# Kernel tuning notes

Measured on AMD Instinct MI355X. Metric: run time of the kernel, lower is better.

Reference implementation:

```python
import jax, jax.numpy as jnp
import numpy as np

WS = 7       # window_size
NH = 4       # num_head = dim_in // dim_head
HD = 64      # dim_head
ALPHA = 0.1
BETA = 0.2
THETA = 0.5
EPS = 1e-5   # LayerNorm eps


def dwconv(x, w):
    # x: [b, C, h, w], w: [C, 1, k, k] depthwise, padding 'same', no bias
    return jax.lax.conv_general_dilated(
        x, w, window_strides=(1, 1), padding='SAME',
        feature_group_count=x.shape[1],
        dimension_numbers=('NCHW', 'OIHW', 'NCHW'))


def setup_inputs() -> dict:
    key = jax.random.key(0)
    ks = jax.random.split(key, 8)
    B, H, W, C = 32, 56, 56, 256
    s = 0.02
    return {
        'x': jax.random.normal(ks[0], (B, H, W, C), jnp.float32),
        'qkv_w': jax.random.normal(ks[1], (3 * C, C), jnp.float32) * s,
        'qkv_b': jnp.zeros((3 * C,), jnp.float32),
        'conv3_w': jax.random.normal(ks[2], (C, 1, 3, 3), jnp.float32) * s,
        'conv5_w': jax.random.normal(ks[3], (C, 1, 5, 5), jnp.float32) * s,
        'conv7_w': jax.random.normal(ks[4], (C, 1, 7, 7), jnp.float32) * s,
        'ffn_in_w': jax.random.normal(ks[5], (C, C), jnp.float32) * s,
        'ffn_out_w': jax.random.normal(ks[6], (C, C), jnp.float32) * s,
        'ln_g': jnp.ones((C,), jnp.float32),
        'ln_b': jnp.zeros((C,), jnp.float32),
    }


def reference(x, qkv_w, qkv_b, conv3_w, conv5_w, conv7_w, ffn_in_w, ffn_out_w, ln_g, ln_b):
    B, H, W, C = x.shape
    n1, n2 = H // WS, W // WS  # H,W divisible by WS -> no padding path
    # rearrange 'b (h1 n1) (w1 n2) c -> (b n1 n2) h1 w1 c' (window dim is MAJOR axis)
    xw = x.reshape(B, WS, n1, WS, n2, C).transpose(0, 2, 4, 1, 3, 5)
    xw = xw.reshape(B * n1 * n2, WS, WS, C)
    b, hw = B * n1 * n2, WS * WS

    shortcut = xw.reshape(b, hw, NH, HD).transpose(0, 2, 1, 3)  # [b, nh, hw, hd]
    qkv = xw.reshape(b, hw, C) @ qkv_w.T + qkv_b                # [b, hw, 3C]
    qkv = qkv.reshape(b, hw, 3, NH, HD).transpose(2, 0, 3, 1, 4)
    q, k, v = qkv[0], qkv[1], qkv[2]
    v = ALPHA * v + shortcut                                     # scaled residual into V
    shortcut2 = v.transpose(0, 2, 1, 3).reshape(b, WS, WS, C)    # [b, h, w, C]

    # SDPA with default scale hd^-0.5
    attn = jax.nn.softmax(jnp.einsum('bnqd,bnkd->bnqk', q, k) * (HD ** -0.5), axis=-1)
    x_spa = jnp.einsum('bnqk,bnkd->bnqd', attn, v)
    x_spa = x_spa.transpose(0, 2, 1, 3).reshape(b, WS, WS, C)

    # conv branches on modified v: v.transpose(-1,-2).reshape(b, C, h, w)
    xc = v.transpose(0, 1, 3, 2).reshape(b, C, WS, WS)
    c3 = dwconv(xc, conv3_w).transpose(0, 2, 3, 1)
    c5 = dwconv(xc, conv5_w).transpose(0, 2, 3, 1)
    c7 = dwconv(xc, conv7_w).transpose(0, 2, 3, 1)
    x_spa = 0.25 * (x_spa + c3 + c5 + c7)  # equal 0.25 branch weights

    xw = BETA * x_spa + shortcut2
    # inverse rearrange '(b n1 n2) h1 w1 c -> b (h1 n1) (w1 n2) c'
    xo = xw.reshape(B, n1, n2, WS, WS, C).transpose(0, 3, 1, 4, 2, 5).reshape(B, H, W, C)

    # FFN (bias=False) with scaled residual, then LayerNorm
    y = jax.nn.silu(xo @ ffn_in_w.T) @ ffn_out_w.T
    xo = THETA * y + xo
    mu = jnp.mean(xo, axis=-1, keepdims=True)
    var = jnp.var(xo, axis=-1, keepdims=True)
    return (xo - mu) / jnp.sqrt(var + EPS) * ln_g + ln_b
```

## Files before the change

### kernel.cpp

```cpp
#include <hip/hip_runtime.h>

typedef unsigned short u16;
typedef unsigned short u16x8 __attribute__((ext_vector_type(8)));
typedef unsigned short u16x4 __attribute__((ext_vector_type(4)));
typedef unsigned int   u32x2 __attribute__((ext_vector_type(2)));
typedef short          s16x8 __attribute__((ext_vector_type(8)));
typedef float          f32x4 __attribute__((ext_vector_type(4)));

#define DEV static __device__ __forceinline__

DEV float bf2f(u16 u){ unsigned int v = ((unsigned int)u) << 16; return __builtin_bit_cast(float, v); }
DEV u16 f2bf(float f){
  unsigned int u = __builtin_bit_cast(unsigned int, f);
  u += 0x7fffu + ((u >> 16) & 1u);
  return (u16)(u >> 16);
}

DEV f32x4 mfma16(u16x8 a, u16x8 b, f32x4 c){
  return __builtin_amdgcn_mfma_f32_16x16x32_bf16(
      __builtin_bit_cast(s16x8, a), __builtin_bit_cast(s16x8, b), c, 0, 0, 0);
}

DEV void g2l16(const void* g, void* l){
  __builtin_amdgcn_global_load_lds((const __attribute__((address_space(1))) void*)g,
                                   (__attribute__((address_space(3))) void*)l, 16, 0, 0);
}

DEV size_t xrow_from(int b, int hw){
  int h1 = hw / 7, w1 = hw - h1 * 7;
  return ((size_t)(((b >> 6) * 56 + h1 * 8 + ((b >> 3) & 7)) * 56 + (w1 * 8 + (b & 7)))) << 8;
}
DEV size_t xrow_off(int t){ int b = t / 49; return xrow_from(b, t - b * 49); }

DEV size_t xo_off(int t, int ch){
  int b = t / 49, hw = t - b * 49;
  return (size_t)b * 12544 + (size_t)((ch >> 7) * 6272) + (size_t)hw * 128 + (ch & 127);
}

__global__ __launch_bounds__(256) void k_prep(const float* __restrict__ qkvw,
                                              const float* __restrict__ c3,
                                              const float* __restrict__ c5,
                                              const float* __restrict__ c7,
                                              const float* __restrict__ fin,
                                              const float* __restrict__ fout,
                                              u16* __restrict__ wq, u16* __restrict__ wfi,
                                              u16* __restrict__ wfo, float* __restrict__ weff){
  int id = blockIdx.x * 256 + threadIdx.x;
  if (id < 196608) { wq[id] = f2bf(qkvw[id]); return; }
  id -= 196608;
  if (id < 65536) { wfi[id] = f2bf(fin[id]); return; }
  id -= 65536;
  if (id < 65536) { wfo[id] = f2bf(fout[id]); return; }
  id -= 65536;
  if (id < 12544) {
    int c = id / 49, t = id - c * 49;
    int di = t / 7 - 3, dj = t % 7 - 3;
    float s = c7[c * 49 + t];
    if (di >= -2 && di <= 2 && dj >= -2 && dj <= 2) s += c5[c * 25 + (di + 2) * 5 + (dj + 2)];
    if (di >= -1 && di <= 1 && dj >= -1 && dj <= 1) s += c3[c * 9 + (di + 1) * 3 + (dj + 1)];
    weff[t * 256 + c] = 0.05f * s;
  }
}

__global__ __launch_bounds__(256) void k_xbf(const float* __restrict__ x, u16* __restrict__ xbf){
  int tid = threadIdx.x;
  int tok = blockIdx.x * 4 + (tid >> 6);
  int c4 = (tid & 63) * 4;
  float4 v = *(const float4*)(x + xrow_off(tok) + c4);
  u16x4 o; o[0] = f2bf(v.x); o[1] = f2bf(v.y); o[2] = f2bf(v.z); o[3] = f2bf(v.w);
  *(u16x4*)&xbf[(size_t)tok * 256 + c4] = o;
}

__global__ __launch_bounds__(256) void k_qkv(const u16* __restrict__ xbf,
                                             const u16* __restrict__ wq,
                                             const float* __restrict__ qkvb,
                                             u16* __restrict__ qb, u16* __restrict__ kb,
                                             u16* __restrict__ vmb){
  __shared__ __align__(16) u16 As[128 * 64];
  __shared__ __align__(16) u16 Bs[128 * 64];
  const int bid = blockIdx.x;
  const int lin = (bid & 7) * 588 + (bid >> 3);
  const int bm = lin / 6, bn = lin - bm * 6;
  const int tid = threadIdx.x, lane = tid & 63, wid = tid >> 6;
  const int wm = wid >> 1, wn = wid & 1;
  const int r = lane & 15, g = lane >> 4;
  const int lr = lane >> 3, l8 = (lane & 7) * 16;
  const f32x4 fz = {0.f, 0.f, 0.f, 0.f};
  f32x4 acc[4][4];
#pragma unroll
  for (int m = 0; m < 4; ++m)
#pragma unroll
    for (int n = 0; n < 4; ++n) acc[m][n] = fz;

  const char* gA0 = (const char*)xbf + (size_t)bm * 128 * 512;
  const char* gB0 = (const char*)wq  + (size_t)bn * 128 * 512;

  for (int kt = 0; kt < 4; ++kt) {
#pragma unroll
    for (int ri = 0; ri < 4; ++ri) {
      int chunk = ri * 4 + wid;
      int row = chunk * 8 + lr;
      g2l16(gA0 + (size_t)row * 512 + kt * 128 + l8, (char*)As + chunk * 1024);
      g2l16(gB0 + (size_t)row * 512 + kt * 128 + l8, (char*)Bs + chunk * 1024);
    }
    __syncthreads();
#pragma unroll
    for (int kk = 0; kk < 2; ++kk) {
      u16x8 af[4], bq[4];
#pragma unroll
      for (int m = 0; m < 4; ++m) af[m] = *(const u16x8*)&As[(wm * 64 + m * 16 + r) * 64 + kk * 32 + g * 8];
#pragma unroll
      for (int n = 0; n < 4; ++n) bq[n] = *(const u16x8*)&Bs[(wn * 64 + n * 16 + r) * 64 + kk * 32 + g * 8];
#pragma unroll
      for (int m = 0; m < 4; ++m)
#pragma unroll
        for (int n = 0; n < 4; ++n) acc[m][n] = mfma16(af[m], bq[n], acc[m][n]);
    }
    __syncthreads();
  }

  const int sec = bn >> 1;
  const int colbase = bn * 128 + wn * 64;
  float bias[4];
#pragma unroll
  for (int n = 0; n < 4; ++n) bias[n] = qkvb[colbase + n * 16 + r];
#pragma unroll
  for (int m = 0; m < 4; ++m) {
#pragma unroll
    for (int i = 0; i < 4; ++i) {
      int t = bm * 128 + wm * 64 + m * 16 + g * 4 + i;
      int b = t / 49, hw = t - b * 49;
      size_t tokbase = (size_t)b * 12544;
#pragma unroll
      for (int n = 0; n < 4; ++n) {
        int col = colbase + n * 16 + r;
        float v = acc[m][n][i] + bias[n];
        if (sec == 0) {
          int c = col;
          qb[tokbase + (size_t)(c >> 6) * 3136 + hw * 64 + (c & 63)] = f2bf(v * 0.125f);
        } else if (sec == 1) {
          int c = col - 256;
          kb[tokbase + (size_t)(c >> 6) * 3136 + hw * 64 + (c & 63)] = f2bf(v);
        } else {
          int c = col - 512;
          float xv = bf2f(xbf[(size_t)t * 256 + c]);
          vmb[tokbase + (size_t)(c >> 6) * 3136 + hw * 64 + (c & 63)] = f2bf(0.1f * v + xv);
        }
      }
    }
  }
}

template<int HW0, int NPIX>
DEV void conv_do(const float (&in_f)[49], const float (&wreg)[49], const u16* xs,
                 int c, size_t obase, u16* __restrict__ xo){
#pragma unroll
  for (int p = 0; p < NPIX; ++p) {
    const int hw = HW0 + p;
    const int i0 = hw / 7, j0 = hw % 7;
    float a = 0.f;
#pragma unroll
    for (int di = -3; di <= 3; ++di) {
      const int ii = i0 + di;
      if (ii < 0 || ii > 6) continue;
#pragma unroll
      for (int dj = -3; dj <= 3; ++dj) {
        const int jj = j0 + dj;
        if (jj < 0 || jj > 6) continue;
        a += in_f[ii * 7 + jj] * wreg[(di + 3) * 7 + (dj + 3)];
      }
    }
    float xsv = bf2f(xs[hw * 72 + c]);
    float outv = in_f[hw] + 0.05f * xsv + a;
    xo[obase + (size_t)hw * 128] = f2bf(outv);
  }
}

__global__ __launch_bounds__(256) void k_attn(const u16* __restrict__ qb,
                                              const u16* __restrict__ kb,
                                              const u16* __restrict__ vmb,
                                              const float* __restrict__ weff,
                                              u16* __restrict__ xo){
  __shared__ __align__(16) u16 smem[2 * 16272];
  const int bx = blockIdx.x;
  const int b = bx >> 1, hp = bx & 1;
  const int tid = threadIdx.x, lane = tid & 63, wid = tid >> 6;
  const int hl = wid >> 1, hf = wid & 1;
  const int hg = hp * 2 + hl;
  const int base = hl * 16272;
  const int qo = base, ko = base + 3528, vto = base + 7056, po = base + 11664;
  const int r = lane & 15, g = lane >> 4;
  const size_t hbase = (size_t)(b * 4 + hg) * 3136;

  if (hf == 1) {
#pragma unroll
    for (int rr = 0; rr < 7; ++rr) {
      int ci = rr * 64 + lane;
      if (ci < 392) {
        int hw = ci >> 3, c16 = ci & 7;
        *(u16x8*)&smem[qo + hw * 72 + c16 * 8] = *(const u16x8*)&qb[hbase + hw * 64 + c16 * 8];
      }
    }
#pragma unroll
    for (int rr = 0; rr < 7; ++rr) {
      int ci = rr * 64 + lane;
      if (ci < 392) {
        int hw = ci >> 3, c16 = ci & 7;
        *(u16x8*)&smem[ko + hw * 72 + c16 * 8] = *(const u16x8*)&kb[hbase + hw * 64 + c16 * 8];
      }
    }
  } else {
    int c = lane;
    u16 pix[49];
#pragma unroll
    for (int hw = 0; hw < 49; ++hw) pix[hw] = vmb[hbase + hw * 64 + c];
#pragma unroll
    for (int t2 = 0; t2 < 12; ++t2) {
      u32x2 w;
      w[0] = (unsigned)pix[4 * t2] | ((unsigned)pix[4 * t2 + 1] << 16);
      w[1] = (unsigned)pix[4 * t2 + 2] | ((unsigned)pix[4 * t2 + 3] << 16);
      *(u32x2*)&smem[vto + c * 72 + 4 * t2] = w;
    }
    u32x2 wl; wl[0] = (unsigned)pix[48]; wl[1] = 0u;
    *(u32x2*)&smem[vto + c * 72 + 48] = wl;
    u32x2 z; z[0] = 0u; z[1] = 0u;
    *(u32x2*)&smem[vto + c * 72 + 52] = z;
    *(u32x2*)&smem[vto + c * 72 + 56] = z;
    *(u32x2*)&smem[vto + c * 72 + 60] = z;
  }
  __syncthreads();

  const int mt0 = hf * 2;
  const f32x4 fz = {0.f, 0.f, 0.f, 0.f};
  f32x4 s[2][4];
#pragma unroll
  for (int m = 0; m < 2; ++m)
#pragma unroll
    for (int n = 0; n < 4; ++n) s[m][n] = fz;
#pragma unroll
  for (int kk = 0; kk < 2; ++kk) {
    u16x8 aq[2], bk[4];
#pragma unroll
    for (int m = 0; m < 2; ++m) aq[m] = *(const u16x8*)&smem[qo + ((mt0 + m) * 16 + r) * 72 + kk * 32 + g * 8];
#pragma unroll
    for (int n = 0; n < 4; ++n) bk[n] = *(const u16x8*)&smem[ko + (n * 16 + r) * 72 + kk * 32 + g * 8];
#pragma unroll
    for (int m = 0; m < 2; ++m)
#pragma unroll
      for (int n = 0; n < 4; ++n) s[m][n] = mfma16(aq[m], bk[n], s[m][n]);
  }

#pragma unroll
  for (int m = 0; m < 2; ++m) {
#pragma unroll
    for (int i = 0; i < 4; ++i) {
      float x0 = s[m][0][i], x1 = s[m][1][i], x2 = s[m][2][i];
      float x3 = (r >= 1) ? -1e30f : s[m][3][i];
      float mx = fmaxf(fmaxf(x0, x1), fmaxf(x2, x3));
#pragma unroll
      for (int off = 1; off < 16; off <<= 1) mx = fmaxf(mx, __shfl_xor(mx, off, 64));
      float e0 = __expf(x0 - mx), e1 = __expf(x1 - mx), e2 = __expf(x2 - mx);
      float e3 = (r >= 1) ? 0.f : __expf(x3 - mx);
      float sum = e0 + e1 + e2 + e3;
#pragma unroll
      for (int off = 1; off < 16; off <<= 1) sum += __shfl_xor(sum, off, 64);
      float inv = 1.f / sum;
      int rowp = po + ((mt0 + m) * 16 + g * 4 + i) * 72;
      smem[rowp + r]       = f2bf(e0 * inv);
      smem[rowp + 16 + r]  = f2bf(e1 * inv);
      smem[rowp + 32 + r]  = f2bf(e2 * inv);
      smem[rowp + 48 + r]  = f2bf(e3 * inv);
    }
  }

  f32x4 o[2][4];
#pragma unroll
  for (int m = 0; m < 2; ++m)
#pragma unroll
    for (int n = 0; n < 4; ++n) o[m][n] = fz;
#pragma unroll
  for (int kk = 0; kk < 2; ++kk) {
    u16x8 pa[2], vb[4];
#pragma unroll
    for (int m = 0; m < 2; ++m) pa[m] = *(const u16x8*)&smem[po + ((mt0 + m) * 16 + r) * 72 + kk * 32 + g * 8];
#pragma unroll
    for (int n = 0; n < 4; ++n) vb[n] = *(const u16x8*)&smem[vto + (n * 16 + r) * 72 + kk * 32 + g * 8];
#pragma unroll
    for (int m = 0; m < 2; ++m)
#pragma unroll
      for (int n = 0; n < 4; ++n) o[m][n] = mfma16(pa[m], vb[n], o[m][n]);
  }
#pragma unroll
  for (int m = 0; m < 2; ++m)
#pragma unroll
    for (int n = 0; n < 4; ++n)
#pragma unroll
      for (int i = 0; i < 4; ++i)
        smem[po + ((mt0 + m) * 16 + g * 4 + i) * 72 + n * 16 + r] = f2bf(o[m][n][i]);
  __syncthreads();

  {
    int c = lane;
    float in_f[49];
#pragma unroll
    for (int t2 = 0; t2 < 6; ++t2) {
      u16x8 raw = *(const u16x8*)&smem[vto + c * 72 + t2 * 8];
#pragma unroll
      for (int e = 0; e < 8; ++e) in_f[t2 * 8 + e] = bf2f(raw[e]);
    }
    in_f[48] = bf2f(smem[vto + c * 72 + 48]);
    float wreg[49];
#pragma unroll
    for (int t2 = 0; t2 < 49; ++t2) wreg[t2] = weff[t2 * 256 + hg * 64 + c];
    size_t obase = (size_t)b * 12544 + (size_t)hp * 6272 + (size_t)(hl * 64 + c);
    if (hf == 0) conv_do<0, 25>(in_f, wreg, &smem[po], c, obase, xo);
    else         conv_do<25, 24>(in_f, wreg, &smem[po], c, obase, xo);
  }
}

__global__ __launch_bounds__(256) void k_ffn1(const u16* __restrict__ xo,
                                              const u16* __restrict__ wfi,
                                              u16* __restrict__ h){
  __shared__ __align__(16) u16 As[128 * 64];
  __shared__ __align__(16) u16 Bs[128 * 64];
  const int bid = blockIdx.x;
  const int lin = (bid & 7) * 196 + (bid >> 3);
  const int bm = lin >> 1, bn = lin & 1;
  const int tid = threadIdx.x, lane = tid & 63, wid = tid >> 6;
  const int wm = wid >> 1, wn = wid & 1;
  const int r = lane & 15, g = lane >> 4;
  const int lr = lane >> 3, l8 = (lane & 7) * 16;
  const f32x4 fz = {0.f, 0.f, 0.f, 0.f};
  f32x4 acc[4][4];
#pragma unroll
  for (int m = 0; m < 4; ++m)
#pragma unroll
    for (int n = 0; n < 4; ++n) acc[m][n] = fz;

  for (int kt = 0; kt < 4; ++kt) {
#pragma unroll
    for (int ri = 0; ri < 4; ++ri) {
      int chunk = ri * 4 + wid;
      int row = chunk * 8 + lr;
      int t = bm * 128 + row;
      int b49 = t / 49, hw = t - b49 * 49;
      size_t off = (size_t)b49 * 12544 + (size_t)(kt >> 1) * 6272 + (size_t)hw * 128 + (kt & 1) * 64;
      g2l16((const char*)xo + off * 2 + l8, (char*)As + chunk * 1024);
      g2l16((const char*)wfi + (size_t)(bn * 128 + row) * 512 + kt * 128 + l8, (char*)Bs + chunk * 1024);
    }
    __syncthreads();
#pragma unroll
    for (int kk = 0; kk < 2; ++kk) {
      u16x8 af[4], bq[4];
#pragma unroll
      for (int m = 0; m < 4; ++m) af[m] = *(const u16x8*)&As[(wm * 64 + m * 16 + r) * 64 + kk * 32 + g * 8];
#pragma unroll
      for (int n = 0; n < 4; ++n) bq[n] = *(const u16x8*)&Bs[(wn * 64 + n * 16 + r) * 64 + kk * 32 + g * 8];
#pragma unroll
      for (int m = 0; m < 4; ++m)
#pragma unroll
        for (int n = 0; n < 4; ++n) acc[m][n] = mfma16(af[m], bq[n], acc[m][n]);
    }
    __syncthreads();
  }
#pragma unroll
  for (int m = 0; m < 4; ++m)
#pragma unroll
    for (int i = 0; i < 4; ++i) {
      int t = bm * 128 + wm * 64 + m * 16 + g * 4 + i;
#pragma unroll
      for (int n = 0; n < 4; ++n) {
        int col = bn * 128 + wn * 64 + n * 16 + r;
        float v = acc[m][n][i];
        float sg = v / (1.f + __expf(-v));
        h[(size_t)t * 256 + col] = f2bf(sg);
      }
    }
}

__global__ __launch_bounds__(512) void k_ffn2(const u16* __restrict__ h,
                                              const u16* __restrict__ wfo,
                                              const u16* __restrict__ xo,
                                              const float* __restrict__ lng,
                                              const float* __restrict__ lnb,
                                              float* __restrict__ out){
  __shared__ __align__(16) u16 As[128 * 64];
  __shared__ __align__(16) u16 Bs[256 * 64];
  __shared__ float red1[4][128];
  __shared__ float red2[4][128];
  const int bm = blockIdx.x;
  const int tid = threadIdx.x, lane = tid & 63, wid = tid >> 6;
  const int wm = wid >> 2, wn = wid & 3;
  const int r = lane & 15, g = lane >> 4;
  const int lr = lane >> 3, l8 = (lane & 7) * 16;
  const f32x4 fz = {0.f, 0.f, 0.f, 0.f};
  f32x4 acc[4][4];
#pragma unroll
  for (int m = 0; m < 4; ++m)
#pragma unroll
    for (int n = 0; n < 4; ++n) acc[m][n] = fz;

  for (int kt = 0; kt < 4; ++kt) {
#pragma unroll
    for (int ri = 0; ri < 2; ++ri) {
      int chunk = ri * 8 + wid;
      int row = chunk * 8 + lr;
      g2l16((const char*)h + (size_t)(bm * 128 + row) * 512 + kt * 128 + l8, (char*)As + chunk * 1024);
    }
#pragma unroll
    for (int ri = 0; ri < 4; ++ri) {
      int chunk = ri * 8 + wid;
      int row = chunk * 8 + lr;
      g2l16((const char*)wfo + (size_t)row * 512 + kt * 128 + l8, (char*)Bs + chunk * 1024);
    }
    __syncthreads();
#pragma unroll
    for (int kk = 0; kk < 2; ++kk) {
      u16x8 af[4], bq[4];
#pragma unroll
      for (int m = 0; m < 4; ++m) af[m] = *(const u16x8*)&As[(wm * 64 + m * 16 + r) * 64 + kk * 32 + g * 8];
#pragma unroll
      for (int n = 0; n < 4; ++n) bq[n] = *(const u16x8*)&Bs[(wn * 64 + n * 16 + r) * 64 + kk * 32 + g * 8];
#pragma unroll
      for (int m = 0; m < 4; ++m)
#pragma unroll
        for (int n = 0; n < 4; ++n) acc[m][n] = mfma16(af[m], bq[n], acc[m][n]);
    }
    __syncthreads();
  }

  float lg[4], lb[4];
#pragma unroll
  for (int n = 0; n < 4; ++n) {
    int col = wn * 64 + n * 16 + r;
    lg[n] = lng[col]; lb[n] = lnb[col];
  }
#pragma unroll
  for (int m = 0; m < 4; ++m)
#pragma unroll
    for (int i = 0; i < 4; ++i) {
      int t = bm * 128 + wm * 64 + m * 16 + g * 4 + i;
      int b49 = t / 49, hw = t - b49 * 49;
      size_t xbase = (size_t)b49 * 12544 + (size_t)hw * 128;
#pragma unroll
      for (int n = 0; n < 4; ++n) {
        int col = wn * 64 + n * 16 + r;
        acc[m][n][i] = 0.5f * acc[m][n][i] + bf2f(xo[xbase + (col >> 7) * 6272 + (col & 127)]);
      }
    }
#pragma unroll
  for (int m = 0; m < 4; ++m)
#pragma unroll
    for (int i = 0; i < 4; ++i) {
      float s1 = 0.f, s2 = 0.f;
#pragma unroll
      for (int n = 0; n < 4; ++n) { float v = acc[m][n][i]; s1 += v; s2 += v * v; }
#pragma unroll
      for (int off = 1; off < 16; off <<= 1) { s1 += __shfl_xor(s1, off, 64); s2 += __shfl_xor(s2, off, 64); }
      if (r == 0) {
        int rl = wm * 64 + m * 16 + g * 4 + i;
        red1[wn][rl] = s1; red2[wn][rl] = s2;
      }
    }
  __syncthreads();
#pragma unroll
  for (int m = 0; m < 4; ++m)
#pragma unroll
    for (int i = 0; i < 4; ++i) {
      int rl = wm * 64 + m * 16 + g * 4 + i;
      float S1 = red1[0][rl] + red1[1][rl] + red1[2][rl] + red1[3][rl];
      float S2 = red2[0][rl] + red2[1][rl] + red2[2][rl] + red2[3][rl];
      float mu = S1 * (1.f / 256.f);
      float var = S2 * (1.f / 256.f) - mu * mu;
      float rstd = rsqrtf(var + 1e-5f);
      int t = bm * 128 + rl;
      int b49 = t / 49, hw = t - b49 * 49;
      size_t ob = xrow_from(b49, hw);
#pragma unroll
      for (int n = 0; n < 4; ++n) {
        int col = wn * 64 + n * 16 + r;
        out[ob + col] = (acc[m][n][i] - mu) * rstd * lg[n] + lb[n];
      }
    }
}

extern "C" void kernel_launch(void* const* d_in, const int* in_sizes, int n_in,
                              void* d_out, int out_size, void* d_ws, size_t ws_size,
                              hipStream_t stream) {
  (void)in_sizes; (void)n_in; (void)out_size; (void)ws_size;
  const float* x     = (const float*)d_in[0];
  const float* qkvw  = (const float*)d_in[1];
  const float* qkvb  = (const float*)d_in[2];
  const float* c3    = (const float*)d_in[3];
  const float* c5    = (const float*)d_in[4];
  const float* c7    = (const float*)d_in[5];
  const float* fin   = (const float*)d_in[6];
  const float* fout  = (const float*)d_in[7];
  const float* lng   = (const float*)d_in[8];
  const float* lnb   = (const float*)d_in[9];
  float* out = (float*)d_out;
  char* ws = (char*)d_ws;

  u16*   qbuf = (u16*)(ws);
  u16*   kbuf = (u16*)(ws + 51380224);
  u16*   vmb  = (u16*)(ws + 102760448);
  u16*   wq   = (u16*)(ws + 154140672);
  u16*   wfi  = (u16*)(ws + 154533888);
  u16*   wfo  = (u16*)(ws + 154664960);
  float* weff = (float*)(ws + 154796032);
  u16*   xbf  = (u16*)d_out;

  k_prep<<<dim3(1329), dim3(256), 0, stream>>>(qkvw, c3, c5, c7, fin, fout, wq, wfi, wfo, weff);
  k_xbf<<<dim3(25088), dim3(256), 0, stream>>>(x, xbf);
  k_qkv<<<dim3(4704), dim3(256), 0, stream>>>(xbf, wq, qkvb, qbuf, kbuf, vmb);
  k_attn<<<dim3(4096), dim3(256), 0, stream>>>(qbuf, kbuf, vmb, weff, kbuf );
  k_ffn1<<<dim3(1568), dim3(256), 0, stream>>>(kbuf , wfi, qbuf );
  k_ffn2<<<dim3(784), dim3(512), 0, stream>>>(qbuf , wfo, kbuf , lng, lnb, out);
}
```

Before: 307.9 us.

## Double-buffer LDS tiles and XOR-swizzle layout in QKV/FFN GEMMs

Adds double-buffered LDS staging with prefetch of the next K tile in the QKV and FFN1 GEMMs, using explicit vmcnt waits and raw barriers so global loads overlap MFMA work. Applies an XOR swizzle to the global-to-LDS copy source offsets and the matching LDS fragment reads in all three GEMMs to reduce LDS bank conflicts. This doubles LDS use per block in two kernels, which may lower occupancy, and relies on hand-counted vmcnt values being correct.

```diff
diff --git a/kernel.cpp b/kernel.cpp
--- a/kernel.cpp
+++ b/kernel.cpp
@@ -31,11 +31,6 @@
   return ((size_t)(((b >> 6) * 56 + h1 * 8 + ((b >> 3) & 7)) * 56 + (w1 * 8 + (b & 7)))) << 8;
 }
 DEV size_t xrow_off(int t){ int b = t / 49; return xrow_from(b, t - b * 49); }
-
-DEV size_t xo_off(int t, int ch){
-  int b = t / 49, hw = t - b * 49;
-  return (size_t)b * 12544 + (size_t)((ch >> 7) * 6272) + (size_t)hw * 128 + (ch & 127);
-}
 
 __global__ __launch_bounds__(256) void k_prep(const float* __restrict__ qkvw,
                                               const float* __restrict__ c3,
@@ -76,15 +71,16 @@
                                              const float* __restrict__ qkvb,
                                              u16* __restrict__ qb, u16* __restrict__ kb,
                                              u16* __restrict__ vmb){
-  __shared__ __align__(16) u16 As[128 * 64];
-  __shared__ __align__(16) u16 Bs[128 * 64];
+  __shared__ __align__(16) u16 As[2][128 * 64];
+  __shared__ __align__(16) u16 Bs[2][128 * 64];
   const int bid = blockIdx.x;
   const int lin = (bid & 7) * 588 + (bid >> 3);
   const int bm = lin / 6, bn = lin - bm * 6;
   const int tid = threadIdx.x, lane = tid & 63, wid = tid >> 6;
   const int wm = wid >> 1, wn = wid & 1;
   const int r = lane & 15, g = lane >> 4;
-  const int lr = lane >> 3, l8 = (lane & 7) * 16;
+  const int lr = lane >> 3;
+  const int swz = ((lane & 7) ^ lr) * 16;
   const f32x4 fz = {0.f, 0.f, 0.f, 0.f};
   f32x4 acc[4][4];
 #pragma unroll
@@ -95,28 +91,42 @@
   const char* gA0 = (const char*)xbf + (size_t)bm * 128 * 512;
   const char* gB0 = (const char*)wq  + (size_t)bn * 128 * 512;
 
-  for (int kt = 0; kt < 4; ++kt) {
+  auto stage = [&](int kt, int buf){
 #pragma unroll
     for (int ri = 0; ri < 4; ++ri) {
       int chunk = ri * 4 + wid;
       int row = chunk * 8 + lr;
-      g2l16(gA0 + (size_t)row * 512 + kt * 128 + l8, (char*)As + chunk * 1024);
-      g2l16(gB0 + (size_t)row * 512 + kt * 128 + l8, (char*)Bs + chunk * 1024);
-    }
-    __syncthreads();
+      g2l16(gA0 + (size_t)row * 512 + kt * 128 + swz, (char*)As[buf] + chunk * 1024);
+      g2l16(gB0 + (size_t)row * 512 + kt * 128 + swz, (char*)Bs[buf] + chunk * 1024);
+    }
+  };
+
+  stage(0, 0);
+#pragma unroll
+  for (int kt = 0; kt < 4; ++kt) {
+    const int cur = kt & 1;
+    if (kt < 3) {
+      stage(kt + 1, cur ^ 1);
+      asm volatile("s_waitcnt vmcnt(8)" ::: "memory");
+    } else {
+      asm volatile("s_waitcnt vmcnt(0)" ::: "memory");
+    }
+    __builtin_amdgcn_s_barrier();
 #pragma unroll
     for (int kk = 0; kk < 2; ++kk) {
       u16x8 af[4], bq[4];
 #pragma unroll
-      for (int m = 0; m < 4; ++m) af[m] = *(const u16x8*)&As[(wm * 64 + m * 16 + r) * 64 + kk * 32 + g * 8];
-#pragma unroll
-      for (int n = 0; n < 4; ++n) bq[n] = *(const u16x8*)&Bs[(wn * 64 + n * 16 + r) * 64 + kk * 32 + g * 8];
-#pragma unroll
       for (int m = 0; m < 4; ++m)
+        af[m] = *(const u16x8*)&As[cur][(wm * 64 + m * 16 + r) * 64 + (((kk * 4 + g) ^ (r & 7)) * 8)];
+#pragma unroll
+      for (int n = 0; n < 4; ++n)
+        bq[n] = *(const u16x8*)&Bs[cur][(wn * 64 + n * 16 + r) * 64 + (((kk * 4 + g) ^ (r & 7)) * 8)];
+#pragma unroll
+      for (int m = 0; m < 4; ++m)
 #pragma unroll
         for (int n = 0; n < 4; ++n) acc[m][n] = mfma16(af[m], bq[n], acc[m][n]);
     }
-    __syncthreads();
+    __builtin_amdgcn_s_barrier();
   }
 
   const int sec = bn >> 1;
@@ -321,15 +331,16 @@
 __global__ __launch_bounds__(256) void k_ffn1(const u16* __restrict__ xo,
                                               const u16* __restrict__ wfi,
                                               u16* __restrict__ h){
-  __shared__ __align__(16) u16 As[128 * 64];
-  __shared__ __align__(16) u16 Bs[128 * 64];
+  __shared__ __align__(16) u16 As[2][128 * 64];
+  __shared__ __align__(16) u16 Bs[2][128 * 64];
   const int bid = blockIdx.x;
   const int lin = (bid & 7) * 196 + (bid >> 3);
   const int bm = lin >> 1, bn = lin & 1;
   const int tid = threadIdx.x, lane = tid & 63, wid = tid >> 6;
   const int wm = wid >> 1, wn = wid & 1;
   const int r = lane & 15, g = lane >> 4;
-  const int lr = lane >> 3, l8 = (lane & 7) * 16;
+  const int lr = lane >> 3;
+  const int swz = ((lane & 7) ^ lr) * 16;
   const f32x4 fz = {0.f, 0.f, 0.f, 0.f};
   f32x4 acc[4][4];
 #pragma unroll
@@ -337,7 +348,7 @@
 #pragma unroll
     for (int n = 0; n < 4; ++n) acc[m][n] = fz;
 
-  for (int kt = 0; kt < 4; ++kt) {
+  auto stage = [&](int kt, int buf){
 #pragma unroll
     for (int ri = 0; ri < 4; ++ri) {
       int chunk = ri * 4 + wid;
@@ -345,23 +356,37 @@
       int t = bm * 128 + row;
       int b49 = t / 49, hw = t - b49 * 49;
       size_t off = (size_t)b49 * 12544 + (size_t)(kt >> 1) * 6272 + (size_t)hw * 128 + (kt & 1) * 64;
-      g2l16((const char*)xo + off * 2 + l8, (char*)As + chunk * 1024);
-      g2l16((const char*)wfi + (size_t)(bn * 128 + row) * 512 + kt * 128 + l8, (char*)Bs + chunk * 1024);
-    }
-    __syncthreads();
+      g2l16((const char*)xo + off * 2 + swz, (char*)As[buf] + chunk * 1024);
+      g2l16((const char*)wfi + (size_t)(bn * 128 + row) * 512 + kt * 128 + swz, (char*)Bs[buf] + chunk * 1024);
+    }
+  };
+
+  stage(0, 0);
+#pragma unroll
+  for (int kt = 0; kt < 4; ++kt) {
+    const int cur = kt & 1;
+    if (kt < 3) {
+      stage(kt + 1, cur ^ 1);
+      asm volatile("s_waitcnt vmcnt(8)" ::: "memory");
+    } else {
+      asm volatile("s_waitcnt vmcnt(0)" ::: "memory");
+    }
+    __builtin_amdgcn_s_barrier();
 #pragma unroll
     for (int kk = 0; kk < 2; ++kk) {
       u16x8 af[4], bq[4];
 #pragma unroll
-      for (int m = 0; m < 4; ++m) af[m] = *(const u16x8*)&As[(wm * 64 + m * 16 + r) * 64 + kk * 32 + g * 8];
-#pragma unroll
-      for (int n = 0; n < 4; ++n) bq[n] = *(const u16x8*)&Bs[(wn * 64 + n * 16 + r) * 64 + kk * 32 + g * 8];
-#pragma unroll
       for (int m = 0; m < 4; ++m)
+        af[m] = *(const u16x8*)&As[cur][(wm * 64 + m * 16 + r) * 64 + (((kk * 4 + g) ^ (r & 7)) * 8)];
+#pragma unroll
+      for (int n = 0; n < 4; ++n)
+        bq[n] = *(const u16x8*)&Bs[cur][(wn * 64 + n * 16 + r) * 64 + (((kk * 4 + g) ^ (r & 7)) * 8)];
+#pragma unroll
+      for (int m = 0; m < 4; ++m)
 #pragma unroll
         for (int n = 0; n < 4; ++n) acc[m][n] = mfma16(af[m], bq[n], acc[m][n]);
     }
-    __syncthreads();
+    __builtin_amdgcn_s_barrier();
   }
 #pragma unroll
   for (int m = 0; m < 4; ++m)
@@ -392,7 +417,8 @@
   const int tid = threadIdx.x, lane = tid & 63, wid = tid >> 6;
   const int wm = wid >> 2, wn = wid & 3;
   const int r = lane & 15, g = lane >> 4;
-  const int lr = lane >> 3, l8 = (lane & 7) * 16;
+  const int lr = lane >> 3;
+  const int swz = ((lane & 7) ^ lr) * 16;
   const f32x4 fz = {0.f, 0.f, 0.f, 0.f};
   f32x4 acc[4][4];
 #pragma unroll
@@ -405,22 +431,24 @@
     for (int ri = 0; ri < 2; ++ri) {
       int chunk = ri * 8 + wid;
       int row = chunk * 8 + lr;
-      g2l16((const char*)h + (size_t)(bm * 128 + row) * 512 + kt * 128 + l8, (char*)As + chunk * 1024);
+      g2l16((const char*)h + (size_t)(bm * 128 + row) * 512 + kt * 128 + swz, (char*)As + chunk * 1024);
     }
 #pragma unroll
     for (int ri = 0; ri < 4; ++ri) {
       int chunk = ri * 8 + wid;
       int row = chunk * 8 + lr;
-      g2l16((const char*)wfo + (size_t)row * 512 + kt * 128 + l8, (char*)Bs + chunk * 1024);
+      g2l16((const char*)wfo + (size_t)row * 512 + kt * 128 + swz, (char*)Bs + chunk * 1024);
     }
     __syncthreads();
 #pragma unroll
     for (int kk = 0; kk < 2; ++kk) {
       u16x8 af[4], bq[4];
 #pragma unroll
-      for (int m = 0; m < 4; ++m) af[m] = *(const u16x8*)&As[(wm * 64 + m * 16 + r) * 64 + kk * 32 + g * 8];
-#pragma unroll
-      for (int n = 0; n < 4; ++n) bq[n] = *(const u16x8*)&Bs[(wn * 64 + n * 16 + r) * 64 + kk * 32 + g * 8];
+      for (int m = 0; m < 4; ++m)
+        af[m] = *(const u16x8*)&As[(wm * 64 + m * 16 + r) * 64 + (((kk * 4 + g) ^ (r & 7)) * 8)];
+#pragma unroll
+      for (int n = 0; n < 4; ++n)
+        bq[n] = *(const u16x8*)&Bs[(wn * 64 + n * 16 + r) * 64 + (((kk * 4 + g) ^ (r & 7)) * 8)];
 #pragma unroll
       for (int m = 0; m < 4; ++m)
 #pragma unroll
```

After: 320.3 us. +4.0%, slower.
